# Kernel optimization log

Measured on AMD Instinct MI355X. Metric: run time of the kernel, lower is better.

The kernel has to match this reference:

```python
import jax, jax.numpy as jnp
import numpy as np

N, E = 50000, 800000
IN_F, HID, OUT_F, K = 128, 128, 64, 3
LAMBDA_MAX = 2.0  # standard upper bound for normalized-Laplacian eigenvalues (dgl.laplacian_lambda_max)
BN_EPS = 1e-5


def setup_inputs() -> dict:
    key = jax.random.key(0)
    ks = jax.random.split(key, 8)
    s = 0.05
    features = jax.random.normal(ks[0], (N, IN_F), jnp.float32)
    src = jax.random.randint(ks[1], (E,), 0, N)
    dst = jax.random.randint(ks[2], (E,), 0, N)
    W1 = jax.random.normal(ks[3], (HID, K * IN_F), jnp.float32) * s
    b1 = jnp.zeros((HID,), jnp.float32)
    W3 = jax.random.normal(ks[4], (HID, K * HID), jnp.float32) * s
    b3 = jnp.zeros((HID,), jnp.float32)
    gamma = jnp.ones((HID,), jnp.float32)
    beta = jnp.zeros((HID,), jnp.float32)
    Wm1 = jax.random.normal(ks[5], (HID, HID), jnp.float32) * s
    bm1 = jnp.zeros((HID,), jnp.float32)
    Wm2 = jax.random.normal(ks[6], (OUT_F, HID), jnp.float32) * s
    bm2 = jnp.zeros((OUT_F,), jnp.float32)
    return dict(features=features, src=src, dst=dst, W1=W1, b1=b1, W3=W3, b3=b3,
                gamma=gamma, beta=beta, Wm1=Wm1, bm1=bm1, Wm2=Wm2, bm2=bm2)


def chebconv(feat, src, dst, d_invsqrt, W, b, k):
    """DGL ChebConv: T_0 = X, T_1 = Lhat X, T_i = 2 Lhat T_{i-1} - T_{i-2};
    Lhat = (2/lam) (I - Ahat) - I, Ahat = D^{-1/2} A D^{-1/2}; linear over concat of orders."""
    re_norm = 2.0 / LAMBDA_MAX
    n = feat.shape[0]

    def spmv(x):  # Ahat @ x via edge gather (src) + segment-sum scatter (dst)
        return jax.ops.segment_sum((x * d_invsqrt)[src], dst, num_segments=n) * d_invsqrt

    Xs = [feat]
    if k > 1:
        h = spmv(feat)
        Xs.append(-re_norm * h + feat * (re_norm - 1.0))
    for _ in range(2, k):
        h = spmv(Xs[-1])
        Xs.append(-2.0 * re_norm * h + Xs[-1] * (2.0 * (re_norm - 1.0)) - Xs[-2])
    return jnp.concatenate(Xs, axis=1) @ W.T + b  # [N, k*d] @ [d_out, k*d]^T


def reference(features, src, dst, W1, b1, W3, b3, gamma, beta, Wm1, bm1, Wm2, bm2):
    n = features.shape[0]
    in_deg = jax.ops.segment_sum(jnp.ones((src.shape[0],), jnp.float32), dst, num_segments=n)
    d_invsqrt = (jnp.clip(in_deg, 1.0, None) ** -0.5)[:, None]

    x = jax.nn.relu(chebconv(features, src, dst, d_invsqrt, W1, b1, K))
    # BatchNorm1d (training-mode batch stats, biased variance)
    mu = x.mean(axis=0)
    var = x.var(axis=0)
    x = (x - mu) * jax.lax.rsqrt(var + BN_EPS) * gamma + beta
    # NOTE: the source's Chebyshev early-stopping loop computes cheb2(x) repeatedly but
    # never reassigns `x`, so it is output-inert and omitted (same math).
    x_res = x
    x = jax.nn.relu(chebconv(x, src, dst, d_invsqrt, W3, b3, K))
    x = x + x_res  # dropout in eval mode == identity
    h = jax.nn.relu(x @ Wm1.T + bm1)
    return h @ Wm2.T + bm2
```

## Files before the change

kernel.cpp:

```cpp
#include <hip/hip_runtime.h>
#include <hip/hip_bf16.h>
#include <math.h>

#define NF 128

typedef __bf16 bf16x8 __attribute__((ext_vector_type(8)));
typedef unsigned short ushort8 __attribute__((ext_vector_type(8)));
typedef float f32x4 __attribute__((ext_vector_type(4)));
typedef _Float16 half8 __attribute__((ext_vector_type(8)));
typedef _Float16 half4 __attribute__((ext_vector_type(4)));

static inline int ceil_div(int a, int b) { return (a + b - 1) / b; }


__global__ __launch_bounds__(256) void bucket_hist_kernel(const int* __restrict__ dst,
                                                          int* __restrict__ counts,
                                                          int e, int nblk, int nbuck) {
  __shared__ int h[256];
  int t = threadIdx.x, blk = blockIdx.x;
  h[t] = 0;
  __syncthreads();
  int base = blk * 4096;
#pragma unroll
  for (int k = 0; k < 16; ++k) {
    int i = base + k * 256 + t;
    if (i < e) atomicAdd(&h[dst[i] >> 8], 1);
  }
  __syncthreads();
  for (int b = t; b < nbuck; b += 256) counts[b * nblk + blk] = h[b];
}

__global__ __launch_bounds__(256) void bucket_scan_rows_kernel(int* __restrict__ counts,
                                                               int* __restrict__ btot,
                                                               int nblk) {
  __shared__ int sh[256];
  int b = blockIdx.x, t = threadIdx.x;
  int* row = counts + (size_t)b * nblk;
  int carry = 0;
  for (int base = 0; base < nblk; base += 256) {
    int v = (base + t < nblk) ? row[base + t] : 0;
    sh[t] = v;
    __syncthreads();
    for (int off = 1; off < 256; off <<= 1) {
      int add = (t >= off) ? sh[t - off] : 0;
      __syncthreads();
      sh[t] += add;
      __syncthreads();
    }
    if (base + t < nblk) row[base + t] = carry + sh[t] - v;
    carry += sh[255];
    __syncthreads();
  }
  if (t == 0) btot[b] = carry;
}

__global__ __launch_bounds__(256) void bucket_base_kernel(const int* __restrict__ btot,
                                                          int* __restrict__ bbase,
                                                          int nbuck, int e) {
  __shared__ int sh[256];
  __shared__ int carry;
  int t = threadIdx.x;
  if (t == 0) carry = 0;
  __syncthreads();
  for (int base = 0; base < nbuck; base += 256) {
    int v = (base + t < nbuck) ? btot[base + t] : 0;
    sh[t] = v;
    __syncthreads();
    for (int off = 1; off < 256; off <<= 1) {
      int add = (t >= off) ? sh[t - off] : 0;
      __syncthreads();
      sh[t] += add;
      __syncthreads();
    }
    if (base + t < nbuck) bbase[base + t] = carry + sh[t] - v;
    __syncthreads();
    if (t == 0) carry += sh[255];
    __syncthreads();
  }
  if (t == 0) bbase[nbuck] = e;
}

__global__ __launch_bounds__(256) void bucket_bin_kernel(const int* __restrict__ src,
                                                         const int* __restrict__ dst,
                                                         const int* __restrict__ counts,
                                                         const int* __restrict__ bbase,
                                                         int2* __restrict__ binned,
                                                         int e, int nblk, int nbuck) {
  __shared__ int cur[256];
  int t = threadIdx.x, blk = blockIdx.x;
  for (int b = t; b < nbuck; b += 256) cur[b] = counts[b * nblk + blk] + bbase[b];
  __syncthreads();
  int base = blk * 4096;
#pragma unroll
  for (int k = 0; k < 16; ++k) {
    int i = base + k * 256 + t;
    if (i < e) {
      int d = dst[i];
      int pos = atomicAdd(&cur[d >> 8], 1);
      binned[pos] = make_int2(src[i], d);
    }
  }
}

__global__ __launch_bounds__(256) void bucket_finalize_kernel(const int2* __restrict__ binned,
                                                              const int* __restrict__ bbase,
                                                              int* __restrict__ offsets,
                                                              int* __restrict__ csr,
                                                              float* __restrict__ dinv,
                                                              int n, int e, int nbuck) {
  __shared__ int deg[256];
  __shared__ int offs[256];
  __shared__ int cur[256];
  int b = blockIdx.x, t = threadIdx.x;
  int ebeg = bbase[b];
  int eend = bbase[b + 1];
  deg[t] = 0;
  __syncthreads();
  for (int j = ebeg + t; j < eend; j += 256) atomicAdd(&deg[binned[j].y & 255], 1);
  __syncthreads();
  int v = deg[t];
  offs[t] = v;
  __syncthreads();
  for (int off = 1; off < 256; off <<= 1) {
    int add = (t >= off) ? offs[t - off] : 0;
    __syncthreads();
    offs[t] += add;
    __syncthreads();
  }
  int excl = offs[t] - v;
  cur[t] = excl;
  int node = b * 256 + t;
  if (node < n) {
    offsets[node] = ebeg + excl;
    float d = (float)(v > 1 ? v : 1);
    dinv[node] = rsqrtf(d);
  }
  if (b == nbuck - 1 && t == 0) offsets[n] = e;
  __syncthreads();
  for (int j = ebeg + t; j < eend; j += 256) {
    int2 pr = binned[j];
    int pos = atomicAdd(&cur[pr.y & 255], 1);
    csr[ebeg + pos] = pr.x;
  }
}

__global__ void scale16_kernel(const float* __restrict__ x, const float* __restrict__ dinv,
                               _Float16* __restrict__ out16, int n) {
  int i = blockIdx.x * 256 + threadIdx.x;
  if (i < n * (NF / 4)) {
    int row = i >> 5;
    float4 v = ((const float4*)x)[i];
    float d = dinv[row];
    half4 h;
    h[0] = (_Float16)(v.x * d); h[1] = (_Float16)(v.y * d);
    h[2] = (_Float16)(v.z * d); h[3] = (_Float16)(v.w * d);
    ((half4*)out16)[i] = h;
  }
}

__global__ __launch_bounds__(256) void spmv_kernel(
    const _Float16* __restrict__ xs16, const float* __restrict__ dinv,
    const int* __restrict__ offsets, const int* __restrict__ csr,
    const float* __restrict__ z, float a, float bz,
    float* __restrict__ out, _Float16* __restrict__ outs16, int n) {
  int w = threadIdx.x >> 6, lane = threadIdx.x & 63;
  int node = blockIdx.x * 4 + w;
  if (node >= n) return;
  int beg = __builtin_amdgcn_readfirstlane(offsets[node]);
  int end = __builtin_amdgcn_readfirstlane(offsets[node + 1]);
  int eh = lane >> 4;
  int cq = lane & 15;

  float acc[8];
#pragma unroll
  for (int j = 0; j < 8; ++j) acc[j] = 0.f;

  int e2 = beg;
  for (; e2 + 8 <= end; e2 += 8) {
    int s0 = csr[e2 + eh];
    int s1 = csr[e2 + 4 + eh];
    half8 g0 = ((const half8*)(xs16 + (size_t)s0 * NF))[cq];
    half8 g1 = ((const half8*)(xs16 + (size_t)s1 * NF))[cq];
#pragma unroll
    for (int j = 0; j < 8; ++j) acc[j] += (float)g0[j];
#pragma unroll
    for (int j = 0; j < 8; ++j) acc[j] += (float)g1[j];
  }
  for (; e2 + 4 <= end; e2 += 4) {
    int s0 = csr[e2 + eh];
    half8 g0 = ((const half8*)(xs16 + (size_t)s0 * NF))[cq];
#pragma unroll
    for (int j = 0; j < 8; ++j) acc[j] += (float)g0[j];
  }
  int rem = end - e2;
  if (eh < rem) {
    int s0 = csr[e2 + eh];
    half8 g0 = ((const half8*)(xs16 + (size_t)s0 * NF))[cq];
#pragma unroll
    for (int j = 0; j < 8; ++j) acc[j] += (float)g0[j];
  }
#pragma unroll
  for (int j = 0; j < 8; ++j) {
    acc[j] += __shfl_xor(acc[j], 16);
    acc[j] += __shfl_xor(acc[j], 32);
  }
  if (eh == 0) {
    float dv = dinv[node];
    float v[8];
#pragma unroll
    for (int j = 0; j < 8; ++j) v[j] = a * dv * acc[j];
    if (z) {
      const f32x4* zp = (const f32x4*)(z + (size_t)node * NF + cq * 8);
      f32x4 z0 = zp[0], z1 = zp[1];
#pragma unroll
      for (int j = 0; j < 4; ++j) { v[j] += bz * z0[j]; v[4 + j] += bz * z1[j]; }
    }
    f32x4 o0, o1;
#pragma unroll
    for (int j = 0; j < 4; ++j) { o0[j] = v[j]; o1[j] = v[4 + j]; }
    f32x4* op = (f32x4*)(out + (size_t)node * NF + cq * 8);
    op[0] = o0; op[1] = o1;
    if (outs16) {
      half8 hv;
#pragma unroll
      for (int j = 0; j < 8; ++j) hv[j] = (_Float16)(v[j] * dv);
      *(half8*)(outs16 + (size_t)node * NF + cq * 8) = hv;
    }
  }
}

__device__ __forceinline__ void pack_one(const float* __restrict__ W, ushort8* __restrict__ Wp,
                                         int f, int NT, int K) {
  int lane = f & 63;
  int hl = (f >> 6) & 1;
  int rest = f >> 7;
  int nt = rest % NT;
  int kunit = rest / NT;
  int nrow = nt * 16 + (lane & 15);
  int k0 = kunit * 32 + (lane >> 4) * 8;
  const float* srcp = W + (size_t)nrow * K + k0;
  ushort8 v;
#pragma unroll
  for (int j = 0; j < 8; ++j) {
    float x = srcp[j];
    __bf16 h = (__bf16)x;
    if (hl) h = (__bf16)(x - (float)h);
    v[j] = __builtin_bit_cast(unsigned short, h);
  }
  Wp[f] = v;
}

__global__ void pack_all_kernel(const float* __restrict__ W1, ushort8* __restrict__ P1,
                                const float* __restrict__ W3, ushort8* __restrict__ P3,
                                const float* __restrict__ Wm1, ushort8* __restrict__ PM1,
                                const float* __restrict__ Wm2, ushort8* __restrict__ PM2) {
  int f = blockIdx.x * 256 + threadIdx.x;
  if (f < 12288) pack_one(W1, P1, f, 8, 384);
  else if (f < 24576) pack_one(W3, P3, f - 12288, 8, 384);
  else if (f < 28672) pack_one(Wm1, PM1, f - 24576, 8, 128);
  else if (f < 30720) pack_one(Wm2, PM2, f - 28672, 4, 128);
}


__device__ __forceinline__ void lds_put_split(unsigned short* AH, unsigned short* AL,
                                              int row, int col, float v) {
  __bf16 hh = (__bf16)v;
  __bf16 ll = (__bf16)(v - (float)hh);
  int off = row * 128 + ((((col >> 3) ^ (row & 15))) << 3) + (col & 7);
  AH[off] = __builtin_bit_cast(unsigned short, hh);
  AL[off] = __builtin_bit_cast(unsigned short, ll);
}

__device__ __forceinline__ void cvt_frag(const float4& a, const float4& b,
                                         float4* AHI, float4* ALO, int idx) {
  float xv[8] = {a.x, a.y, a.z, a.w, b.x, b.y, b.z, b.w};
  ushort8 hi, lo;
#pragma unroll
  for (int j = 0; j < 8; ++j) {
    __bf16 hh = (__bf16)xv[j];
    __bf16 ll = (__bf16)(xv[j] - (float)hh);
    hi[j] = __builtin_bit_cast(unsigned short, hh);
    lo[j] = __builtin_bit_cast(unsigned short, ll);
  }
  AHI[idx] = __builtin_bit_cast(float4, hi);
  ALO[idx] = __builtin_bit_cast(float4, lo);
}

template<int NT, int NT2>
__device__ __forceinline__ void gemm_step512(const float4* AHI, const float4* ALO,
                                             const ushort8* __restrict__ Wp, int kunit,
                                             int lane, int wm, int wn, f32x4 (*acc)[NT2]) {
  bf16x8 ah[2], al[2];
#pragma unroll
  for (int mt = 0; mt < 2; ++mt) {
    int arow = wm * 32 + mt * 16 + (lane & 15);
    int fc = (kunit & 3) * 4 + (lane >> 4);
    int idx = arow * 16 + (fc ^ (arow & 15));
    ah[mt] = __builtin_bit_cast(bf16x8, AHI[idx]);
    al[mt] = __builtin_bit_cast(bf16x8, ALO[idx]);
  }
#pragma unroll
  for (int j = 0; j < NT2; ++j) {
    int nt = wn * NT2 + j;
    const ushort8* bp = Wp + (size_t)(kunit * NT + nt) * 2 * 64 + lane;
    bf16x8 bh = __builtin_bit_cast(bf16x8, bp[0]);
    bf16x8 bl = __builtin_bit_cast(bf16x8, bp[64]);
#pragma unroll
    for (int mt = 0; mt < 2; ++mt) {
      acc[mt][j] = __builtin_amdgcn_mfma_f32_16x16x32_bf16(ah[mt], bh, acc[mt][j], 0, 0, 0);
      acc[mt][j] = __builtin_amdgcn_mfma_f32_16x16x32_bf16(ah[mt], bl, acc[mt][j], 0, 0, 0);
      acc[mt][j] = __builtin_amdgcn_mfma_f32_16x16x32_bf16(al[mt], bh, acc[mt][j], 0, 0, 0);
    }
  }
}

__global__ __launch_bounds__(512) void conv1_gemm_kernel(
    const float* __restrict__ X0, const float* __restrict__ X1, const float* __restrict__ X2,
    const ushort8* __restrict__ Wp, const float* __restrict__ bias,
    float* __restrict__ out, float* __restrict__ stats, int n) {
  __shared__ float4 AHI[1024];
  __shared__ float4 ALO[1024];
  __shared__ float sstat[256];

  int tid = threadIdx.x;
  int lane = tid & 63, wid = tid >> 6;
  int wm = wid >> 2, wn = wid & 3;
  int r0 = blockIdx.x * 64;

  f32x4 acc[2][2];
#pragma unroll
  for (int mt = 0; mt < 2; ++mt)
#pragma unroll
    for (int j = 0; j < 2; ++j) acc[mt][j] = (f32x4)0.f;

  const float* Xarr[3] = {X0, X1, X2};
  float4 pa0[2], pa1[2];
#pragma unroll
  for (int h = 0; h < 2; ++h) {
    int f = tid + h * 512, row = f >> 4, fc = f & 15, grow = r0 + row;
    float4 z = make_float4(0.f, 0.f, 0.f, 0.f);
    pa0[h] = z; pa1[h] = z;
    if (grow < n) {
      const float4* s = (const float4*)(X0 + (size_t)grow * NF + fc * 8);
      pa0[h] = s[0]; pa1[h] = s[1];
    }
  }
#pragma unroll
  for (int p = 0; p < 3; ++p) {
#pragma unroll
    for (int h = 0; h < 2; ++h) {
      int f = tid + h * 512, row = f >> 4, fc = f & 15;
      cvt_frag(pa0[h], pa1[h], AHI, ALO, row * 16 + (fc ^ (row & 15)));
    }
    if (p + 1 < 3) {
      const float* Xn = Xarr[p + 1];
#pragma unroll
      for (int h = 0; h < 2; ++h) {
        int f = tid + h * 512, row = f >> 4, fc = f & 15, grow = r0 + row;
        if (grow < n) {
          const float4* s = (const float4*)(Xn + (size_t)grow * NF + fc * 8);
          pa0[h] = s[0]; pa1[h] = s[1];
        }
      }
    }
    __syncthreads();
#pragma unroll
    for (int ks = 0; ks < 4; ++ks)
      gemm_step512<8, 2>(AHI, ALO, Wp, p * 4 + ks, lane, wm, wn, acc);
    __syncthreads();
  }
  if (tid < 256) sstat[tid] = 0.f;
  __syncthreads();
#pragma unroll
  for (int mt = 0; mt < 2; ++mt) {
    int rbase = r0 + wm * 32 + mt * 16 + (lane >> 4) * 4;
#pragma unroll
    for (int j = 0; j < 2; ++j) {
      int col = wn * 32 + j * 16 + (lane & 15);
      float b = bias[col];
      float sj = 0.f, qj = 0.f;
#pragma unroll
      for (int i = 0; i < 4; ++i) {
        int row = rbase + i;
        if (row < n) {
          float v = fmaxf(acc[mt][j][i] + b, 0.f);
          out[(size_t)row * NF + col] = v;
          sj += v; qj += v * v;
        }
      }
      sj += __shfl_xor(sj, 16); sj += __shfl_xor(sj, 32);
      qj += __shfl_xor(qj, 16); qj += __shfl_xor(qj, 32);
      if ((lane >> 4) == 0) {
        atomicAdd(&sstat[col], sj);
        atomicAdd(&sstat[128 + col], qj);
      }
    }
  }
  __syncthreads();
  if (tid < 256) atomicAdd(&stats[tid], sstat[tid]);
}

__global__ __launch_bounds__(512) void fused_tail_kernel(
    const float* __restrict__ X, const float* __restrict__ T1, const float* __restrict__ T2,
    const ushort8* __restrict__ Wp3, const float* __restrict__ b3,
    const ushort8* __restrict__ WpM1, const float* __restrict__ bm1,
    const ushort8* __restrict__ WpM2, const float* __restrict__ bm2,
    float* __restrict__ out, int n) {
  __shared__ float4 AHI[1024];
  __shared__ float4 ALO[1024];
  unsigned short* AHu = (unsigned short*)AHI;
  unsigned short* ALu = (unsigned short*)ALO;

  int tid = threadIdx.x;
  int lane = tid & 63, wid = tid >> 6;
  int wm = wid >> 2, wn = wid & 3;
  int r0 = blockIdx.x * 64;

  f32x4 acc[2][2];
#pragma unroll
  for (int mt = 0; mt < 2; ++mt)
#pragma unroll
    for (int j = 0; j < 2; ++j) acc[mt][j] = (f32x4)0.f;

  const float* Xarr[3] = {X, T1, T2};
  float4 pa0[2], pa1[2];
#pragma unroll
  for (int h = 0; h < 2; ++h) {
    int f = tid + h * 512, row = f >> 4, fc = f & 15, grow = r0 + row;
    float4 z = make_float4(0.f, 0.f, 0.f, 0.f);
    pa0[h] = z; pa1[h] = z;
    if (grow < n) {
      const float4* s = (const float4*)(X + (size_t)grow * NF + fc * 8);
      pa0[h] = s[0]; pa1[h] = s[1];
    }
  }
#pragma unroll
  for (int p = 0; p < 3; ++p) {
#pragma unroll
    for (int h = 0; h < 2; ++h) {
      int f = tid + h * 512, row = f >> 4, fc = f & 15;
      cvt_frag(pa0[h], pa1[h], AHI, ALO, row * 16 + (fc ^ (row & 15)));
    }
    if (p + 1 < 3) {
      const float* Xn = Xarr[p + 1];
#pragma unroll
      for (int h = 0; h < 2; ++h) {
        int f = tid + h * 512, row = f >> 4, fc = f & 15, grow = r0 + row;
        if (grow < n) {
          const float4* s = (const float4*)(Xn + (size_t)grow * NF + fc * 8);
          pa0[h] = s[0]; pa1[h] = s[1];
        }
      }
    }
    __syncthreads();
#pragma unroll
    for (int ks = 0; ks < 4; ++ks)
      gemm_step512<8, 2>(AHI, ALO, Wp3, p * 4 + ks, lane, wm, wn, acc);
    __syncthreads();
  }
#pragma unroll
  for (int mt = 0; mt < 2; ++mt) {
    int rb = wm * 32 + mt * 16 + (lane >> 4) * 4;
#pragma unroll
    for (int j = 0; j < 2; ++j) {
      int col = wn * 32 + j * 16 + (lane & 15);
      float b = b3[col];
#pragma unroll
      for (int i = 0; i < 4; ++i) {
        int lrow = rb + i;
        int row = r0 + lrow;
        float v = 0.f;
        if (row < n) v = fmaxf(acc[mt][j][i] + b, 0.f) + X[(size_t)row * NF + col];
        lds_put_split(AHu, ALu, lrow, col, v);
      }
    }
  }
  __syncthreads();
  f32x4 acc2[2][2];
#pragma unroll
  for (int mt = 0; mt < 2; ++mt)
#pragma unroll
    for (int j = 0; j < 2; ++j) acc2[mt][j] = (f32x4)0.f;
#pragma unroll
  for (int ks = 0; ks < 4; ++ks)
    gemm_step512<8, 2>(AHI, ALO, WpM1, ks, lane, wm, wn, acc2);
  __syncthreads();
#pragma unroll
  for (int mt = 0; mt < 2; ++mt) {
    int rb = wm * 32 + mt * 16 + (lane >> 4) * 4;
#pragma unroll
    for (int j = 0; j < 2; ++j) {
      int col = wn * 32 + j * 16 + (lane & 15);
      float b = bm1[col];
#pragma unroll
      for (int i = 0; i < 4; ++i) {
        float v = fmaxf(acc2[mt][j][i] + b, 0.f);
        lds_put_split(AHu, ALu, rb + i, col, v);
      }
    }
  }
  __syncthreads();
  f32x4 acc3[2][1];
#pragma unroll
  for (int mt = 0; mt < 2; ++mt) acc3[mt][0] = (f32x4)0.f;
#pragma unroll
  for (int ks = 0; ks < 4; ++ks)
    gemm_step512<4, 1>(AHI, ALO, WpM2, ks, lane, wm, wn, acc3);
#pragma unroll
  for (int mt = 0; mt < 2; ++mt) {
    int rb = wm * 32 + mt * 16 + (lane >> 4) * 4;
    int col = wn * 16 + (lane & 15);
    float b = bm2[col];
#pragma unroll
    for (int i = 0; i < 4; ++i) {
      int row = r0 + rb + i;
      if (row < n) out[(size_t)row * 64 + col] = acc3[mt][0][i] + b;
    }
  }
}

__global__ void bn_scale_kernel(const float* __restrict__ stats, const float* __restrict__ gamma,
                                const float* __restrict__ beta, float* __restrict__ sc,
                                float* __restrict__ sh, float n) {
  int c = threadIdx.x;
  float mu = stats[c] / n;
  float var = stats[NF + c] / n - mu * mu;
  float s = gamma[c] * rsqrtf(var + 1e-5f);
  sc[c] = s;
  sh[c] = beta[c] - mu * s;
}

__global__ void bn_apply_kernel(float* __restrict__ x, const float* __restrict__ sc,
                                const float* __restrict__ sh, const float* __restrict__ dinv,
                                _Float16* __restrict__ xs16, int n) {
  int i = blockIdx.x * 256 + threadIdx.x;
  if (i < n * (NF / 4)) {
    int row = i >> 5;
    int c0 = (i & 31) * 4;
    float4 v = ((const float4*)x)[i];
    v.x = v.x * sc[c0 + 0] + sh[c0 + 0];
    v.y = v.y * sc[c0 + 1] + sh[c0 + 1];
    v.z = v.z * sc[c0 + 2] + sh[c0 + 2];
    v.w = v.w * sc[c0 + 3] + sh[c0 + 3];
    ((float4*)x)[i] = v;
    float d = dinv[row];
    half4 h;
    h[0] = (_Float16)(v.x * d); h[1] = (_Float16)(v.y * d);
    h[2] = (_Float16)(v.z * d); h[3] = (_Float16)(v.w * d);
    ((half4*)xs16)[i] = h;
  }
}

extern "C" void kernel_launch(void* const* d_in, const int* in_sizes, int n_in,
                              void* d_out, int out_size, void* d_ws, size_t ws_size,
                              hipStream_t stream) {
  const float* feat  = (const float*)d_in[0];
  const int*   src   = (const int*)d_in[1];
  const int*   dst   = (const int*)d_in[2];
  const float* W1    = (const float*)d_in[3];
  const float* b1    = (const float*)d_in[4];
  const float* W3    = (const float*)d_in[5];
  const float* b3    = (const float*)d_in[6];
  const float* gamma = (const float*)d_in[7];
  const float* beta  = (const float*)d_in[8];
  const float* Wm1   = (const float*)d_in[9];
  const float* bm1   = (const float*)d_in[10];
  const float* Wm2   = (const float*)d_in[11];
  const float* bm2   = (const float*)d_in[12];
  int n = in_sizes[0] / NF;
  int e = in_sizes[1];

  char* p = (char*)d_ws;
  auto alloc = [&](size_t bytes) {
    char* r = p;
    p += (bytes + 255) & ~size_t(255);
    return r;
  };
  int nblk  = ceil_div(e, 4096);
  int nbuck = ceil_div(n, 256);

  float* dinv     = (float*)alloc((size_t)n * 4);
  int*   offsets  = (int*)alloc((size_t)(n + 1) * 4);
  int*   counts   = (int*)alloc((size_t)nblk * nbuck * 4);
  int*   btot     = (int*)alloc((size_t)nbuck * 4);
  int*   bbase    = (int*)alloc((size_t)(nbuck + 1) * 4);
  int*   csr      = (int*)alloc((size_t)e * 4);
  float* stats    = (float*)alloc(256 * 4);
  float* bnsc     = (float*)alloc(128 * 4);
  float* bnsh     = (float*)alloc(128 * 4);
  ushort8* Wp1  = (ushort8*)alloc(12 * 8 * 2 * 64 * 16);
  ushort8* Wp3  = (ushort8*)alloc(12 * 8 * 2 * 64 * 16);
  ushort8* WpM1 = (ushort8*)alloc(4 * 8 * 2 * 64 * 16);
  ushort8* WpM2 = (ushort8*)alloc(4 * 4 * 2 * 64 * 16);
  size_t matb = (size_t)n * NF * 4;
  float* T1 = (float*)alloc(matb);
  float* T2 = (float*)alloc(matb);
  float* X  = (float*)alloc(matb);
  _Float16* xsA  = (_Float16*)alloc((size_t)n * NF * 2);
  _Float16* xsB  = (_Float16*)alloc((size_t)n * NF * 2);
  int2* binned = (int2*)T2;

  hipMemsetAsync(stats, 0, 256 * 4, stream);

  int fb = ceil_div(n * (NF / 4), 256);
  int sb = ceil_div(n, 4);
  int gb = ceil_div(n, 64);

  bucket_hist_kernel<<<nblk, 256, 0, stream>>>(dst, counts, e, nblk, nbuck);
  bucket_scan_rows_kernel<<<nbuck, 256, 0, stream>>>(counts, btot, nblk);
  bucket_base_kernel<<<1, 256, 0, stream>>>(btot, bbase, nbuck, e);
  bucket_bin_kernel<<<nblk, 256, 0, stream>>>(src, dst, counts, bbase, binned, e, nblk, nbuck);
  bucket_finalize_kernel<<<nbuck, 256, 0, stream>>>(binned, bbase, offsets, csr, dinv, n, e, nbuck);

  pack_all_kernel<<<120, 256, 0, stream>>>(W1, Wp1, W3, Wp3, Wm1, WpM1, Wm2, WpM2);

  scale16_kernel<<<fb, 256, 0, stream>>>(feat, dinv, xsA, n);
  spmv_kernel<<<sb, 256, 0, stream>>>(xsA, dinv, offsets, csr, nullptr, -1.f, 0.f, T1, xsB, n);
  spmv_kernel<<<sb, 256, 0, stream>>>(xsB, dinv, offsets, csr, feat, -2.f, -1.f, T2, nullptr, n);
  conv1_gemm_kernel<<<gb, 512, 0, stream>>>(feat, T1, T2, Wp1, b1, X, stats, n);

  bn_scale_kernel<<<1, 128, 0, stream>>>(stats, gamma, beta, bnsc, bnsh, (float)n);
  bn_apply_kernel<<<fb, 256, 0, stream>>>(X, bnsc, bnsh, dinv, xsA, n);

  spmv_kernel<<<sb, 256, 0, stream>>>(xsA, dinv, offsets, csr, nullptr, -1.f, 0.f, T1, xsB, n);
  spmv_kernel<<<sb, 256, 0, stream>>>(xsB, dinv, offsets, csr, X, -2.f, -1.f, T2, nullptr, n);

  fused_tail_kernel<<<gb, 512, 0, stream>>>(X, T1, T2, Wp3, b3, WpM1, bm1, WpM2, bm2,
                                            (float*)d_out, n);
}
```

Baseline: 300.8 us.

## Store GEMM operands pre-split bf16 and stage them with async global-to-LDS loads

The SpMV, feature-prep and BN-apply kernels now write their outputs as pre-swizzled bf16 hi/lo split rows instead of fp32. The GEMM kernels then copy these tiles straight into LDS with double-buffered global_load_lds calls, with no per-block fp32 loads or conversion. The same bytes per element are written and read, but the conversion work and register staging leave the GEMM kernels and the global-to-LDS copy can overlap compute. The cost is extra split work in the producer kernels and an added dependence on hand-written vmcnt waits being correct.

After: 305.4 us. About the same (+1.5%).

```diff
diff --git a/kernel.cpp b/kernel.cpp
--- a/kernel.cpp
+++ b/kernel.cpp
@@ -11,7 +11,6 @@
 typedef _Float16 half4 __attribute__((ext_vector_type(4)));
 
 static inline int ceil_div(int a, int b) { return (a + b - 1) / b; }
-
 
 __global__ __launch_bounds__(256) void bucket_hist_kernel(const int* __restrict__ dst,
                                                           int* __restrict__ counts,
@@ -144,25 +143,42 @@
   }
 }
 
-__global__ void scale16_kernel(const float* __restrict__ x, const float* __restrict__ dinv,
-                               _Float16* __restrict__ out16, int n) {
+__device__ __forceinline__ void split8(const float* xv, ushort8& hi, ushort8& lo) {
+#pragma unroll
+  for (int j = 0; j < 8; ++j) {
+    __bf16 hh = (__bf16)xv[j];
+    __bf16 ll = (__bf16)(xv[j] - (float)hh);
+    hi[j] = __builtin_bit_cast(unsigned short, hh);
+    lo[j] = __builtin_bit_cast(unsigned short, ll);
+  }
+}
+
+__global__ void prep_feat_kernel(const float* __restrict__ feat, const float* __restrict__ dinv,
+                                 unsigned short* __restrict__ Fsp, _Float16* __restrict__ xs,
+                                 int n) {
   int i = blockIdx.x * 256 + threadIdx.x;
-  if (i < n * (NF / 4)) {
-    int row = i >> 5;
-    float4 v = ((const float4*)x)[i];
-    float d = dinv[row];
-    half4 h;
-    h[0] = (_Float16)(v.x * d); h[1] = (_Float16)(v.y * d);
-    h[2] = (_Float16)(v.z * d); h[3] = (_Float16)(v.w * d);
-    ((half4*)out16)[i] = h;
-  }
+  if (i >= n * 16) return;
+  int row = i >> 4, fc = i & 15;
+  const float4* s = (const float4*)(feat + (size_t)row * NF + fc * 8);
+  float4 a = s[0], b = s[1];
+  float xv[8] = {a.x, a.y, a.z, a.w, b.x, b.y, b.z, b.w};
+  float d = dinv[row];
+  half8 h;
+#pragma unroll
+  for (int j = 0; j < 8; ++j) h[j] = (_Float16)(xv[j] * d);
+  *(half8*)(xs + (size_t)row * NF + fc * 8) = h;
+  ushort8 hi, lo;
+  split8(xv, hi, lo);
+  int swz = (fc ^ (row & 15)) * 8;
+  *(ushort8*)(Fsp + (size_t)row * 256 + swz) = hi;
+  *(ushort8*)(Fsp + (size_t)row * 256 + 128 + swz) = lo;
 }
 
 __global__ __launch_bounds__(256) void spmv_kernel(
     const _Float16* __restrict__ xs16, const float* __restrict__ dinv,
     const int* __restrict__ offsets, const int* __restrict__ csr,
     const float* __restrict__ z, float a, float bz,
-    float* __restrict__ out, _Float16* __restrict__ outs16, int n) {
+    unsigned short* __restrict__ outsp, _Float16* __restrict__ outs16, int n) {
   int w = threadIdx.x >> 6, lane = threadIdx.x & 63;
   int node = blockIdx.x * 4 + w;
   if (node >= n) return;
@@ -215,11 +231,11 @@
 #pragma unroll
       for (int j = 0; j < 4; ++j) { v[j] += bz * z0[j]; v[4 + j] += bz * z1[j]; }
     }
-    f32x4 o0, o1;
-#pragma unroll
-    for (int j = 0; j < 4; ++j) { o0[j] = v[j]; o1[j] = v[4 + j]; }
-    f32x4* op = (f32x4*)(out + (size_t)node * NF + cq * 8);
-    op[0] = o0; op[1] = o1;
+    ushort8 hi, lo;
+    split8(v, hi, lo);
+    int swz = (cq ^ (node & 15)) * 8;
+    *(ushort8*)(outsp + (size_t)node * 256 + swz) = hi;
+    *(ushort8*)(outsp + (size_t)node * 256 + 128 + swz) = lo;
     if (outs16) {
       half8 hv;
 #pragma unroll
@@ -262,42 +278,38 @@
 }
 
 
-__device__ __forceinline__ void lds_put_split(unsigned short* AH, unsigned short* AL,
-                                              int row, int col, float v) {
+__device__ __forceinline__ void stage_sp(const unsigned short* gsrc, float4* lbuf, int tid) {
+  const char* g = (const char*)gsrc;
+  char* l = (char*)lbuf;
+#pragma unroll
+  for (int k = 0; k < 4; ++k) {
+    int off = k * 8192 + tid * 16;
+    __builtin_amdgcn_global_load_lds(
+        (const __attribute__((address_space(1))) void*)(g + off),
+        (__attribute__((address_space(3))) void*)(l + off), 16, 0, 0);
+  }
+}
+
+__device__ __forceinline__ void lds_put_split(unsigned short* L, int row, int col, float v) {
   __bf16 hh = (__bf16)v;
   __bf16 ll = (__bf16)(v - (float)hh);
-  int off = row * 128 + ((((col >> 3) ^ (row & 15))) << 3) + (col & 7);
-  AH[off] = __builtin_bit_cast(unsigned short, hh);
-  AL[off] = __builtin_bit_cast(unsigned short, ll);
-}
-
-__device__ __forceinline__ void cvt_frag(const float4& a, const float4& b,
-                                         float4* AHI, float4* ALO, int idx) {
-  float xv[8] = {a.x, a.y, a.z, a.w, b.x, b.y, b.z, b.w};
-  ushort8 hi, lo;
-#pragma unroll
-  for (int j = 0; j < 8; ++j) {
-    __bf16 hh = (__bf16)xv[j];
-    __bf16 ll = (__bf16)(xv[j] - (float)hh);
-    hi[j] = __builtin_bit_cast(unsigned short, hh);
-    lo[j] = __builtin_bit_cast(unsigned short, ll);
-  }
-  AHI[idx] = __builtin_bit_cast(float4, hi);
-  ALO[idx] = __builtin_bit_cast(float4, lo);
+  int base = row * 256 + (((col >> 3) ^ (row & 15)) << 3) + (col & 7);
+  L[base] = __builtin_bit_cast(unsigned short, hh);
+  L[base + 128] = __builtin_bit_cast(unsigned short, ll);
 }
 
 template<int NT, int NT2>
-__device__ __forceinline__ void gemm_step512(const float4* AHI, const float4* ALO,
-                                             const ushort8* __restrict__ Wp, int kunit,
-                                             int lane, int wm, int wn, f32x4 (*acc)[NT2]) {
+__device__ __forceinline__ void gemm_step512(const float4* B4, const ushort8* __restrict__ Wp,
+                                             int kunit, int lane, int wm, int wn,
+                                             f32x4 (*acc)[NT2]) {
   bf16x8 ah[2], al[2];
 #pragma unroll
   for (int mt = 0; mt < 2; ++mt) {
     int arow = wm * 32 + mt * 16 + (lane & 15);
     int fc = (kunit & 3) * 4 + (lane >> 4);
-    int idx = arow * 16 + (fc ^ (arow & 15));
-    ah[mt] = __builtin_bit_cast(bf16x8, AHI[idx]);
-    al[mt] = __builtin_bit_cast(bf16x8, ALO[idx]);
+    int idx = arow * 32 + (fc ^ (arow & 15));
+    ah[mt] = __builtin_bit_cast(bf16x8, B4[idx]);
+    al[mt] = __builtin_bit_cast(bf16x8, B4[idx + 16]);
   }
 #pragma unroll
   for (int j = 0; j < NT2; ++j) {
@@ -314,18 +326,40 @@
   }
 }
 
+__device__ __forceinline__ void gemm3_pipeline(const unsigned short* A0, const unsigned short* A1,
+                                               const unsigned short* A2, const ushort8* Wp,
+                                               float4 (*buf)[2048], size_t r0,
+                                               int tid, int lane, int wm, int wn,
+                                               f32x4 (*acc)[2]) {
+  const unsigned short* Aarr[3] = {A0, A1, A2};
+  stage_sp(A0 + r0 * 256, buf[0], tid);
+#pragma unroll
+  for (int p = 0; p < 3; ++p) {
+    if (p + 1 < 3) stage_sp(Aarr[p + 1] + r0 * 256, buf[(p + 1) & 1], tid);
+    if (p < 2) asm volatile("s_waitcnt vmcnt(4)" ::: "memory");
+    else       asm volatile("s_waitcnt vmcnt(0)" ::: "memory");
+    __builtin_amdgcn_s_barrier();
+    __builtin_amdgcn_sched_barrier(0);
+#pragma unroll
+    for (int ks = 0; ks < 4; ++ks)
+      gemm_step512<8, 2>(buf[p & 1], Wp, p * 4 + ks, lane, wm, wn, acc);
+    __builtin_amdgcn_sched_barrier(0);
+    __builtin_amdgcn_s_barrier();
+  }
+}
+
 __global__ __launch_bounds__(512) void conv1_gemm_kernel(
-    const float* __restrict__ X0, const float* __restrict__ X1, const float* __restrict__ X2,
+    const unsigned short* __restrict__ A0, const unsigned short* __restrict__ A1,
+    const unsigned short* __restrict__ A2,
     const ushort8* __restrict__ Wp, const float* __restrict__ bias,
     float* __restrict__ out, float* __restrict__ stats, int n) {
-  __shared__ float4 AHI[1024];
-  __shared__ float4 ALO[1024];
+  __shared__ float4 buf[2][2048];
   __shared__ float sstat[256];
 
   int tid = threadIdx.x;
   int lane = tid & 63, wid = tid >> 6;
   int wm = wid >> 2, wn = wid & 3;
-  int r0 = blockIdx.x * 64;
+  size_t r0 = (size_t)blockIdx.x * 64;
 
   f32x4 acc[2][2];
 #pragma unroll
@@ -333,47 +367,13 @@
 #pragma unroll
     for (int j = 0; j < 2; ++j) acc[mt][j] = (f32x4)0.f;
 
-  const float* Xarr[3] = {X0, X1, X2};
-  float4 pa0[2], pa1[2];
-#pragma unroll
-  for (int h = 0; h < 2; ++h) {
-    int f = tid + h * 512, row = f >> 4, fc = f & 15, grow = r0 + row;
-    float4 z = make_float4(0.f, 0.f, 0.f, 0.f);
-    pa0[h] = z; pa1[h] = z;
-    if (grow < n) {
-      const float4* s = (const float4*)(X0 + (size_t)grow * NF + fc * 8);
-      pa0[h] = s[0]; pa1[h] = s[1];
-    }
-  }
-#pragma unroll
-  for (int p = 0; p < 3; ++p) {
-#pragma unroll
-    for (int h = 0; h < 2; ++h) {
-      int f = tid + h * 512, row = f >> 4, fc = f & 15;
-      cvt_frag(pa0[h], pa1[h], AHI, ALO, row * 16 + (fc ^ (row & 15)));
-    }
-    if (p + 1 < 3) {
-      const float* Xn = Xarr[p + 1];
-#pragma unroll
-      for (int h = 0; h < 2; ++h) {
-        int f = tid + h * 512, row = f >> 4, fc = f & 15, grow = r0 + row;
-        if (grow < n) {
-          const float4* s = (const float4*)(Xn + (size_t)grow * NF + fc * 8);
-          pa0[h] = s[0]; pa1[h] = s[1];
-        }
-      }
-    }
-    __syncthreads();
-#pragma unroll
-    for (int ks = 0; ks < 4; ++ks)
-      gemm_step512<8, 2>(AHI, ALO, Wp, p * 4 + ks, lane, wm, wn, acc);
-    __syncthreads();
-  }
+  gemm3_pipeline(A0, A1, A2, Wp, buf, r0, tid, lane, wm, wn, acc);
+
   if (tid < 256) sstat[tid] = 0.f;
   __syncthreads();
 #pragma unroll
   for (int mt = 0; mt < 2; ++mt) {
-    int rbase = r0 + wm * 32 + mt * 16 + (lane >> 4) * 4;
+    int rbase = (int)r0 + wm * 32 + mt * 16 + (lane >> 4) * 4;
 #pragma unroll
     for (int j = 0; j < 2; ++j) {
       int col = wn * 32 + j * 16 + (lane & 15);
@@ -401,20 +401,19 @@
 }
 
 __global__ __launch_bounds__(512) void fused_tail_kernel(
-    const float* __restrict__ X, const float* __restrict__ T1, const float* __restrict__ T2,
+    const unsigned short* __restrict__ Xsp, const unsigned short* __restrict__ T1sp,
+    const unsigned short* __restrict__ T2sp, const float* __restrict__ X,
     const ushort8* __restrict__ Wp3, const float* __restrict__ b3,
     const ushort8* __restrict__ WpM1, const float* __restrict__ bm1,
     const ushort8* __restrict__ WpM2, const float* __restrict__ bm2,
     float* __restrict__ out, int n) {
-  __shared__ float4 AHI[1024];
-  __shared__ float4 ALO[1024];
-  unsigned short* AHu = (unsigned short*)AHI;
-  unsigned short* ALu = (unsigned short*)ALO;
+  __shared__ float4 buf[2][2048];
+  unsigned short* L = (unsigned short*)buf[0];
 
   int tid = threadIdx.x;
   int lane = tid & 63, wid = tid >> 6;
   int wm = wid >> 2, wn = wid & 3;
-  int r0 = blockIdx.x * 64;
+  size_t r0 = (size_t)blockIdx.x * 64;
 
   f32x4 acc[2][2];
 #pragma unroll
@@ -422,42 +421,8 @@
 #pragma unroll
     for (int j = 0; j < 2; ++j) acc[mt][j] = (f32x4)0.f;
 
-  const float* Xarr[3] = {X, T1, T2};
-  float4 pa0[2], pa1[2];
-#pragma unroll
-  for (int h = 0; h < 2; ++h) {
-    int f = tid + h * 512, row = f >> 4, fc = f & 15, grow = r0 + row;
-    float4 z = make_float4(0.f, 0.f, 0.f, 0.f);
-    pa0[h] = z; pa1[h] = z;
-    if (grow < n) {
-      const float4* s = (const float4*)(X + (size_t)grow * NF + fc * 8);
-      pa0[h] = s[0]; pa1[h] = s[1];
-    }
-  }
-#pragma unroll
-  for (int p = 0; p < 3; ++p) {
-#pragma unroll
-    for (int h = 0; h < 2; ++h) {
-      int f = tid + h * 512, row = f >> 4, fc = f & 15;
-      cvt_frag(pa0[h], pa1[h], AHI, ALO, row * 16 + (fc ^ (row & 15)));
-    }
-    if (p + 1 < 3) {
-      const float* Xn = Xarr[p + 1];
-#pragma unroll
-      for (int h = 0; h < 2; ++h) {
-        int f = tid + h * 512, row = f >> 4, fc = f & 15, grow = r0 + row;
-        if (grow < n) {
-          const float4* s = (const float4*)(Xn + (size_t)grow * NF + fc * 8);
-          pa0[h] = s[0]; pa1[h] = s[1];
-        }
-      }
-    }
-    __syncthreads();
-#pragma unroll
-    for (int ks = 0; ks < 4; ++ks)
-      gemm_step512<8, 2>(AHI, ALO, Wp3, p * 4 + ks, lane, wm, wn, acc);
-    __syncthreads();
-  }
+  gemm3_pipeline(Xsp, T1sp, T2sp, Wp3, buf, r0, tid, lane, wm, wn, acc);
+
 #pragma unroll
   for (int mt = 0; mt < 2; ++mt) {
     int rb = wm * 32 + mt * 16 + (lane >> 4) * 4;
@@ -468,10 +433,10 @@
 #pragma unroll
       for (int i = 0; i < 4; ++i) {
         int lrow = rb + i;
-        int row = r0 + lrow;
+        int row = (int)r0 + lrow;
         float v = 0.f;
         if (row < n) v = fmaxf(acc[mt][j][i] + b, 0.f) + X[(size_t)row * NF + col];
-        lds_put_split(AHu, ALu, lrow, col, v);
+        lds_put_split(L, lrow, col, v);
       }
     }
   }
@@ -483,7 +448,7 @@
     for (int j = 0; j < 2; ++j) acc2[mt][j] = (f32x4)0.f;
 #pragma unroll
   for (int ks = 0; ks < 4; ++ks)
-    gemm_step512<8, 2>(AHI, ALO, WpM1, ks, lane, wm, wn, acc2);
+    gemm_step512<8, 2>(buf[0], WpM1, ks, lane, wm, wn, acc2);
   __syncthreads();
 #pragma unroll
   for (int mt = 0; mt < 2; ++mt) {
@@ -495,7 +460,7 @@
 #pragma unroll
       for (int i = 0; i < 4; ++i) {
         float v = fmaxf(acc2[mt][j][i] + b, 0.f);
-        lds_put_split(AHu, ALu, rb + i, col, v);
+        lds_put_split(L, rb + i, col, v);
       }
     }
   }
@@ -505,7 +470,7 @@
   for (int mt = 0; mt < 2; ++mt) acc3[mt][0] = (f32x4)0.f;
 #pragma unroll
   for (int ks = 0; ks < 4; ++ks)
-    gemm_step512<4, 1>(AHI, ALO, WpM2, ks, lane, wm, wn, acc3);
+    gemm_step512<4, 1>(buf[0], WpM2, ks, lane, wm, wn, acc3);
 #pragma unroll
   for (int mt = 0; mt < 2; ++mt) {
     int rb = wm * 32 + mt * 16 + (lane >> 4) * 4;
@@ -513,7 +478,7 @@
     float b = bm2[col];
 #pragma unroll
     for (int i = 0; i < 4; ++i) {
-      int row = r0 + rb + i;
+      int row = (int)r0 + rb + i;
       if (row < n) out[(size_t)row * 64 + col] = acc3[mt][0][i] + b;
     }
   }
@@ -532,23 +497,31 @@
 
 __global__ void bn_apply_kernel(float* __restrict__ x, const float* __restrict__ sc,
                                 const float* __restrict__ sh, const float* __restrict__ dinv,
-                                _Float16* __restrict__ xs16, int n) {
+                                unsigned short* __restrict__ Xsp, _Float16* __restrict__ xs16,
+                                int n) {
   int i = blockIdx.x * 256 + threadIdx.x;
-  if (i < n * (NF / 4)) {
-    int row = i >> 5;
-    int c0 = (i & 31) * 4;
-    float4 v = ((const float4*)x)[i];
-    v.x = v.x * sc[c0 + 0] + sh[c0 + 0];
-    v.y = v.y * sc[c0 + 1] + sh[c0 + 1];
-    v.z = v.z * sc[c0 + 2] + sh[c0 + 2];
-    v.w = v.w * sc[c0 + 3] + sh[c0 + 3];
-    ((float4*)x)[i] = v;
-    float d = dinv[row];
-    half4 h;
-    h[0] = (_Float16)(v.x * d); h[1] = (_Float16)(v.y * d);
-    h[2] = (_Float16)(v.z * d); h[3] = (_Float16)(v.w * d);
-    ((half4*)xs16)[i] = h;
-  }
+  if (i >= n * 16) return;
+  int row = i >> 4, fc = i & 15;
+  float4* xp = (float4*)(x + (size_t)row * NF + fc * 8);
+  float4 a = xp[0], b = xp[1];
+  float xv[8] = {a.x, a.y, a.z, a.w, b.x, b.y, b.z, b.w};
+  int c0 = fc * 8;
+#pragma unroll
+  for (int j = 0; j < 8; ++j) xv[j] = xv[j] * sc[c0 + j] + sh[c0 + j];
+  float4 o0, o1;
+  o0.x = xv[0]; o0.y = xv[1]; o0.z = xv[2]; o0.w = xv[3];
+  o1.x = xv[4]; o1.y = xv[5]; o1.z = xv[6]; o1.w = xv[7];
+  xp[0] = o0; xp[1] = o1;
+  float d = dinv[row];
+  half8 h;
+#pragma unroll
+  for (int j = 0; j < 8; ++j) h[j] = (_Float16)(xv[j] * d);
+  *(half8*)(xs16 + (size_t)row * NF + fc * 8) = h;
+  ushort8 hi, lo;
+  split8(xv, hi, lo);
+  int swz = (fc ^ (row & 15)) * 8;
+  *(ushort8*)(Xsp + (size_t)row * 256 + swz) = hi;
+  *(ushort8*)(Xsp + (size_t)row * 256 + 128 + swz) = lo;
 }
 
 extern "C" void kernel_launch(void* const* d_in, const int* in_sizes, int n_in,
@@ -592,17 +565,19 @@
   ushort8* Wp3  = (ushort8*)alloc(12 * 8 * 2 * 64 * 16);
   ushort8* WpM1 = (ushort8*)alloc(4 * 8 * 2 * 64 * 16);
   ushort8* WpM2 = (ushort8*)alloc(4 * 4 * 2 * 64 * 16);
-  size_t matb = (size_t)n * NF * 4;
-  float* T1 = (float*)alloc(matb);
-  float* T2 = (float*)alloc(matb);
-  float* X  = (float*)alloc(matb);
-  _Float16* xsA  = (_Float16*)alloc((size_t)n * NF * 2);
-  _Float16* xsB  = (_Float16*)alloc((size_t)n * NF * 2);
-  int2* binned = (int2*)T2;
+  size_t spb = (size_t)(n + 64) * 512;
+  unsigned short* Fsp  = (unsigned short*)alloc(spb);
+  unsigned short* T1sp = (unsigned short*)alloc(spb);
+  unsigned short* T2sp = (unsigned short*)alloc(spb);
+  unsigned short* Xsp  = (unsigned short*)alloc(spb);
+  float* X = (float*)alloc((size_t)n * NF * 4);
+  _Float16* xsA = (_Float16*)alloc((size_t)n * NF * 2);
+  _Float16* xsB = (_Float16*)alloc((size_t)n * NF * 2);
+  int2* binned = (int2*)Fsp;
 
   hipMemsetAsync(stats, 0, 256 * 4, stream);
 
-  int fb = ceil_div(n * (NF / 4), 256);
+  int fb = ceil_div(n * 16, 256);
   int sb = ceil_div(n, 4);
   int gb = ceil_div(n, 64);
 
@@ -614,17 +589,17 @@
 
   pack_all_kernel<<<120, 256, 0, stream>>>(W1, Wp1, W3, Wp3, Wm1, WpM1, Wm2, WpM2);
 
-  scale16_kernel<<<fb, 256, 0, stream>>>(feat, dinv, xsA, n);
-  spmv_kernel<<<sb, 256, 0, stream>>>(xsA, dinv, offsets, csr, nullptr, -1.f, 0.f, T1, xsB, n);
-  spmv_kernel<<<sb, 256, 0, stream>>>(xsB, dinv, offsets, csr, feat, -2.f, -1.f, T2, nullptr, n);
-  conv1_gemm_kernel<<<gb, 512, 0, stream>>>(feat, T1, T2, Wp1, b1, X, stats, n);
+  prep_feat_kernel<<<fb, 256, 0, stream>>>(feat, dinv, Fsp, xsA, n);
+  spmv_kernel<<<sb, 256, 0, stream>>>(xsA, dinv, offsets, csr, nullptr, -1.f, 0.f, T1sp, xsB, n);
+  spmv_kernel<<<sb, 256, 0, stream>>>(xsB, dinv, offsets, csr, feat, -2.f, -1.f, T2sp, nullptr, n);
+  conv1_gemm_kernel<<<gb, 512, 0, stream>>>(Fsp, T1sp, T2sp, Wp1, b1, X, stats, n);
 
   bn_scale_kernel<<<1, 128, 0, stream>>>(stats, gamma, beta, bnsc, bnsh, (float)n);
-  bn_apply_kernel<<<fb, 256, 0, stream>>>(X, bnsc, bnsh, dinv, xsA, n);
-
-  spmv_kernel<<<sb, 256, 0, stream>>>(xsA, dinv, offsets, csr, nullptr, -1.f, 0.f, T1, xsB, n);
-  spmv_kernel<<<sb, 256, 0, stream>>>(xsB, dinv, offsets, csr, X, -2.f, -1.f, T2, nullptr, n);
-
-  fused_tail_kernel<<<gb, 512, 0, stream>>>(X, T1, T2, Wp3, b3, WpM1, bm1, WpM2, bm2,
+  bn_apply_kernel<<<fb, 256, 0, stream>>>(X, bnsc, bnsh, dinv, Xsp, xsA, n);
+
+  spmv_kernel<<<sb, 256, 0, stream>>>(xsA, dinv, offsets, csr, nullptr, -1.f, 0.f, T1sp, xsB, n);
+  spmv_kernel<<<sb, 256, 0, stream>>>(xsB, dinv, offsets, csr, X, -2.f, -1.f, T2sp, nullptr, n);
+
+  fused_tail_kernel<<<gb, 512, 0, stream>>>(Xsp, T1sp, T2sp, X, Wp3, b3, WpM1, bm1, WpM2, bm2,
                                             (float*)d_out, n);
 }
```
